# Optimization experiments

Hardware: AMD Instinct MI355X
Metric: run time of the kernel (lower is better)

Reference implementation:

```python
import jax, jax.numpy as jnp
import numpy as np

N = 160000   # active voxels
C = 64       # embed_channels
K = 2048     # clusters per level
G = 128      # voxel grid side (grid_size)
NEG = 0.01   # LeakyReLU negative slope (torch default)
EPS_BN = 1e-5


def _build_neighbors():
    # Random unique active voxels in a G^3 grid; 27-neighborhood index map for SubMConv3d.
    rng = np.random.default_rng(0)
    codes = np.sort(rng.choice(G ** 3, size=N, replace=False))
    xc = codes // (G * G); yc = (codes // G) % G; zc = codes % G
    nbrs = []
    for dx in (-1, 0, 1):
        for dy in (-1, 0, 1):
            for dz in (-1, 0, 1):
                nx, ny, nz = xc + dx, yc + dy, zc + dz
                inb = (nx >= 0) & (nx < G) & (ny >= 0) & (ny < G) & (nz >= 0) & (nz < G)
                ncode = nx * (G * G) + ny * G + nz
                pos = np.searchsorted(codes, np.where(inb, ncode, 0))
                pos = np.clip(pos, 0, N - 1)
                found = inb & (codes[pos] == ncode)
                nbrs.append(np.where(found, pos, -1))
    return np.stack(nbrs).astype(np.int32)  # [27, N], -1 = no active neighbor


def setup_inputs():
    key = jax.random.key(0)
    def nrm(i, shape, s=0.05):
        return jax.random.normal(jax.random.fold_in(key, i), shape, jnp.float32) * s
    return {
        'feat': jax.random.normal(jax.random.fold_in(key, 0), (N, C), jnp.float32),
        'lw_W': nrm(1, (3, C, C)), 'lw_g': jnp.ones((3, C)), 'lw_b': jnp.zeros((3, C)),
        'w_W': nrm(2, (3, C, C)),
        'proj_W': nrm(3, (4, C, C)), 'proj_g': jnp.ones((4, C)), 'proj_b': jnp.zeros((4, C)),
        'adaptive_W': nrm(4, (C, 3)),
        'fuse_W': nrm(5, (2 * C, C)), 'fuse_g': jnp.ones((C,)), 'fuse_b': jnp.zeros((C,)),
        'conv1_W': nrm(6, (27, C, C)), 'bn1_g': jnp.ones((C,)), 'bn1_b': jnp.zeros((C,)),
        'conv2_W': nrm(7, (27, C, C)), 'bn2_g': jnp.ones((C,)), 'bn2_b': jnp.zeros((C,)),
        'clusters': jax.random.randint(jax.random.fold_in(key, 8), (3, N), 0, K, dtype=jnp.int32),
        'nbr': jnp.asarray(_build_neighbors()),
    }


def _bn(x, g, b):
    # BatchNorm1d, training-mode (biased batch stats over N)
    m = x.mean(0)
    v = x.var(0)
    return (x - m) * jax.lax.rsqrt(v + EPS_BN) * g + b


def _lrelu(x):
    return jax.nn.leaky_relu(x, NEG)


def _seg_sum(x, seg):
    return jax.ops.segment_sum(x, seg, num_segments=K)


def _subm_conv(f, nbr, W):
    # Submanifold 3x3x3 conv: per kernel offset, masked gather + [C,C] matmul.
    out = jnp.zeros((f.shape[0], W.shape[-1]), f.dtype)
    for k in range(27):
        idx = nbr[k]
        g = jnp.where((idx >= 0)[:, None], f[jnp.maximum(idx, 0)], 0.0)
        out = out + g @ W[k]
    return out


def reference(feat, lw_W, lw_g, lw_b, w_W, proj_W, proj_g, proj_b, adaptive_W,
              fuse_W, fuse_g, fuse_b, conv1_W, bn1_g, bn1_b, conv2_W, bn2_g, bn2_b,
              clusters, nbr):
    feats = []
    for i in range(3):  # depth-1 cluster levels
        c = clusters[i]
        cnt = jnp.clip(_seg_sum(jnp.ones((feat.shape[0], 1), feat.dtype), c), 1.0, None)
        pw = _lrelu(_bn(feat @ lw_W[i], lw_g[i], lw_b[i]))
        pw = pw - (_seg_sum(pw, c) / cnt)[c]          # center by cluster mean
        pw = pw @ w_W[i]
        pw = jnp.exp(pw - pw.max())                    # global-max-stabilized exp
        pw = pw / (_seg_sum(pw, c)[c] + 1e-6)          # per-cluster softmax
        pfeat = _lrelu(_bn(feat @ proj_W[i], proj_g[i], proj_b[i])) * pw
        feats.append(_seg_sum(pfeat, c)[c])            # pool then broadcast back
    adp = jax.nn.softmax(feat @ adaptive_W, axis=1)    # [N, 3]
    feats = jnp.stack(feats, axis=1)                   # [N, 3, C]
    feats = jnp.einsum('ln,lnc->lc', adp, feats)
    f = _lrelu(_bn(feat @ proj_W[3], proj_g[3], proj_b[3]))
    f = jnp.concatenate([f, feats], axis=1)
    f = _lrelu(_bn(f @ fuse_W, fuse_g, fuse_b)) + feat
    res = f
    v = _lrelu(_bn(_subm_conv(f, nbr, conv1_W), bn1_g, bn1_b))
    v = _bn(_subm_conv(v, nbr, conv2_W), bn2_g, bn2_b)
    return _lrelu(v + res)
```

## Files before the change

### kernel.cpp

```cpp
#include <hip/hip_runtime.h>
#include <hip/hip_bf16.h>
#include <math.h>

#define KCL 2048
#define LRELU_NEG 0.01f
#define EPSBN 1e-5f

using s8v = __attribute__((ext_vector_type(8))) short;
using f4v = __attribute__((ext_vector_type(4))) float;

union U8 { ushort u[8]; uint4 v; };

__device__ __forceinline__ float lrelu(float x) { return x > 0.f ? x : LRELU_NEG * x; }
__device__ __forceinline__ ushort f2bf(float f) {
    __hip_bfloat16 h = __float2bfloat16(f);
    return *reinterpret_cast<ushort*>(&h);
}
__device__ __forceinline__ float bf2f(ushort u) { return __uint_as_float(((unsigned)u) << 16); }

__device__ __forceinline__ unsigned encf(float f) {
    unsigned u = __float_as_uint(f);
    return (u & 0x80000000u) ? ~u : (u | 0x80000000u);
}
__device__ __forceinline__ float decf(unsigned u) {
    return __uint_as_float((u & 0x80000000u) ? (u & 0x7fffffffu) : ~u);
}

__device__ __forceinline__ void bn_sb(const double* __restrict__ stats, const float* __restrict__ g,
                                      const float* __restrict__ b, int n, float* sb) {
    int t = threadIdx.x;
    if (t < 64) {
        float mean = (float)(stats[t] / n);
        float ex2 = (float)(stats[64 + t] / n);
        float var = fmaxf(ex2 - mean * mean, 0.f);
        float rstd = rsqrtf(var + EPSBN);
        float sc = rstd * g[t];
        sb[t] = sc;
        sb[64 + t] = b[t] - mean * sc;
    }
    __syncthreads();
}

__device__ __forceinline__ void mfma_tile(const uint4* As, const uint4* Ws, int rowA0, int rowA1,
                                          int swA0, int swA1, int l15, int lg, f4v acc[2][4]) {
    const s8v* Av = (const s8v*)As;
    const s8v* Wv = (const s8v*)Ws;
#pragma unroll
    for (int kb = 0; kb < 2; ++kb) {
        int gch = kb * 4 + lg;
        s8v a0 = Av[rowA0 * 8 + (gch ^ swA0)];
        s8v a1 = Av[rowA1 * 8 + (gch ^ swA1)];
#pragma unroll
        for (int nf = 0; nf < 4; ++nf) {
            int col = nf * 16 + l15;
            s8v bf = Wv[col * 8 + (gch ^ (col & 7))];
            acc[0][nf] = __builtin_amdgcn_mfma_f32_16x16x32_bf16(a0, bf, acc[0][nf], 0, 0, 0);
            acc[1][nf] = __builtin_amdgcn_mfma_f32_16x16x32_bf16(a1, bf, acc[1][nf], 0, 0, 0);
        }
    }
}

__device__ __forceinline__ void stage_w(const ushort* Wmat, uint4* Ws, int wrow, int wq) {
    const uint4* src = (const uint4*)(Wmat + (size_t)wrow * 64);
    int sw = wrow & 7;
    Ws[wrow * 8 + (wq ^ sw)] = src[wq];
    Ws[wrow * 8 + ((wq + 4) ^ sw)] = src[wq + 4];
}

__device__ __forceinline__ void stage_a_bf16(const ushort* S, uint4* As, int row, int n, int arow, int ah) {
    uint4 c0 = {0, 0, 0, 0}, c1 = c0, c2 = c0, c3 = c0;
    if (row < n) {
        const uint4* s = (const uint4*)(S + (size_t)row * 64) + ah * 4;
        c0 = s[0]; c1 = s[1]; c2 = s[2]; c3 = s[3];
    }
    int sw = arow & 7;
    uint4* dst = As + arow * 8;
    dst[(ah * 4 + 0) ^ sw] = c0;
    dst[(ah * 4 + 1) ^ sw] = c1;
    dst[(ah * 4 + 2) ^ sw] = c2;
    dst[(ah * 4 + 3) ^ sw] = c3;
}

__device__ __forceinline__ void stage_a_vals(const float* vals, uint4* As, int arow, int ah) {
    int sw = arow & 7;
    uint4* dst = As + arow * 8;
#pragma unroll
    for (int c = 0; c < 4; ++c) {
        U8 u;
#pragma unroll
        for (int e = 0; e < 8; ++e) u.u[e] = f2bf(vals[c * 8 + e]);
        dst[(ah * 4 + c) ^ sw] = u.v;
    }
}

__global__ __launch_bounds__(256) void prep_wt64(const float* __restrict__ lw, const float* __restrict__ wW,
                                                 const float* __restrict__ proj, const float* __restrict__ c1,
                                                 const float* __restrict__ c2, ushort* __restrict__ wt) {
    int bk = blockIdx.x;
    const float* W;
    if (bk < 3) W = lw + (size_t)bk * 4096;
    else if (bk < 6) W = wW + (size_t)(bk - 3) * 4096;
    else if (bk < 10) W = proj + (size_t)(bk - 6) * 4096;
    else if (bk < 37) W = c1 + (size_t)(bk - 10) * 4096;
    else W = c2 + (size_t)(bk - 37) * 4096;
    ushort* o = wt + (size_t)bk * 4096;
    for (int i = threadIdx.x; i < 4096; i += 256) {
        int kk = i >> 6, cc = i & 63;
        o[cc * 64 + kk] = f2bf(W[i]);
    }
}

__global__ __launch_bounds__(256) void prep_fuse(const float* __restrict__ Wf, ushort* __restrict__ o) {
    for (int i = threadIdx.x; i < 8192; i += 256) {
        int kk = i >> 6, cc = i & 63;
        o[cc * 128 + kk] = f2bf(Wf[i]);
    }
}

__global__ __launch_bounds__(256) void cvt_bf16_kernel(const float* __restrict__ in, ushort* __restrict__ o,
                                                       long n4) {
    for (long i = (long)blockIdx.x * 256 + threadIdx.x; i < n4; i += (long)gridDim.x * 256) {
        float4 x = ((const float4*)in)[i];
        ushort4 u;
        u.x = f2bf(x.x); u.y = f2bf(x.y); u.z = f2bf(x.z); u.w = f2bf(x.w);
        ((ushort4*)o)[i] = u;
    }
}

__global__ __launch_bounds__(256) void hist3_kernel(const int* __restrict__ clusters, int* __restrict__ cnt,
                                                    int n) {
    __shared__ int h[KCL];
    int l = blockIdx.x % 3;
    int nb = gridDim.x / 3, bi = blockIdx.x / 3;
    for (int i = threadIdx.x; i < KCL; i += 256) h[i] = 0;
    __syncthreads();
    const int* cl = clusters + (size_t)l * n;
    for (long i = (long)bi * 256 + threadIdx.x; i < n; i += (long)nb * 256)
        atomicAdd(&h[cl[i]], 1);
    __syncthreads();
    for (int i = threadIdx.x; i < KCL; i += 256) {
        int v = h[i];
        if (v) atomicAdd(&cnt[l * KCL + i], v);
    }
}

__global__ __launch_bounds__(256) void scan_kernel(const int* __restrict__ cnt, int* __restrict__ off,
                                                   int* __restrict__ cursor, int n) {
    int l = blockIdx.x;
    const int* c = cnt + l * KCL;
    __shared__ int part[256];
    __shared__ int pref[256];
    int t = threadIdx.x;
    int base = t * 8;
    int v[8];
    int s = 0;
#pragma unroll
    for (int j = 0; j < 8; ++j) { v[j] = c[base + j]; s += v[j]; }
    part[t] = s;
    __syncthreads();
    if (t == 0) {
        int acc = 0;
        for (int i = 0; i < 256; ++i) { pref[i] = acc; acc += part[i]; }
    }
    __syncthreads();
    int acc = pref[t] + l * n;
#pragma unroll
    for (int j = 0; j < 8; ++j) {
        off[l * KCL + base + j] = acc;
        cursor[l * KCL + base + j] = acc;
        acc += v[j];
    }
}

__global__ __launch_bounds__(256) void scatter_kernel(const int* __restrict__ clusters, int* __restrict__ cursor,
                                                      int* __restrict__ perm, int n) {
    long n3 = (long)n * 3;
    for (long i = (long)blockIdx.x * 256 + threadIdx.x; i < n3; i += (long)gridDim.x * 256) {
        int l = (i >= n) + (i >= 2 * (long)n);
        int c = clusters[i];
        int pos = atomicAdd(&cursor[l * KCL + c], 1);
        perm[pos] = (int)(i - (long)l * n);
    }
}

__global__ __launch_bounds__(256) void adp_kernel(const ushort* __restrict__ feat16, const float* __restrict__ aW,
                                                  float* __restrict__ adp, int n) {
    __shared__ float w[192];
    for (int i = threadIdx.x; i < 192; i += 256) w[i] = aW[i];
    __syncthreads();
    for (long row = (long)blockIdx.x * 256 + threadIdx.x; row < n; row += (long)gridDim.x * 256) {
        const ushort4* fr = (const ushort4*)(feat16 + row * 64);
        float l0 = 0.f, l1 = 0.f, l2 = 0.f;
#pragma unroll
        for (int q = 0; q < 16; ++q) {
            ushort4 uv = fr[q];
            float x0 = bf2f(uv.x), x1 = bf2f(uv.y), x2 = bf2f(uv.z), x3 = bf2f(uv.w);
            int k = q * 4;
            l0 += x0 * w[k * 3 + 0] + x1 * w[k * 3 + 3] + x2 * w[k * 3 + 6] + x3 * w[k * 3 + 9];
            l1 += x0 * w[k * 3 + 1] + x1 * w[k * 3 + 4] + x2 * w[k * 3 + 7] + x3 * w[k * 3 + 10];
            l2 += x0 * w[k * 3 + 2] + x1 * w[k * 3 + 5] + x2 * w[k * 3 + 8] + x3 * w[k * 3 + 11];
        }
        float m = fmaxf(l0, fmaxf(l1, l2));
        float e0 = expf(l0 - m), e1 = expf(l1 - m), e2 = expf(l2 - m);
        float inv = 1.f / (e0 + e1 + e2);
        adp[row * 3 + 0] = e0 * inv;
        adp[row * 3 + 1] = e1 * inv;
        adp[row * 3 + 2] = e2 * inv;
    }
}

__global__ __launch_bounds__(256) void lw3_gemm(const ushort* __restrict__ feat16, const ushort* __restrict__ lwW16,
                                                ushort* __restrict__ A3, int n, double* __restrict__ stats) {
    __shared__ uint4 As[128 * 8];
    __shared__ uint4 Ws[64 * 8];
    __shared__ float red[512];
    int t = threadIdx.x, lane = t & 63, w = t >> 6;
    int rb = blockIdx.x * 128;
    int arow = t >> 1, ah = t & 1;
    int wrow = t >> 2, wq = t & 3;
    const int l15 = lane & 15, lg = lane >> 4;
    int rowA0 = w * 32 + l15, rowA1 = rowA0 + 16;
    int swA0 = rowA0 & 7, swA1 = rowA1 & 7;
    int base = rb + w * 32;

    stage_a_bf16(feat16, As, rb + arow, n, arow, ah);

    for (int j = 0; j < 3; ++j) {
        stage_w(lwW16 + (size_t)j * 4096, Ws, wrow, wq);
        __syncthreads();
        f4v acc[2][4];
#pragma unroll
        for (int rf = 0; rf < 2; ++rf)
#pragma unroll
            for (int nf = 0; nf < 4; ++nf)
#pragma unroll
                for (int q = 0; q < 4; ++q) acc[rf][nf][q] = 0.f;
        mfma_tile(As, Ws, rowA0, rowA1, swA0, swA1, l15, lg, acc);
        ushort* out = A3 + (size_t)j * n * 64;
#pragma unroll
        for (int rf = 0; rf < 2; ++rf)
#pragma unroll
            for (int nf = 0; nf < 4; ++nf)
#pragma unroll
                for (int q = 0; q < 4; ++q) {
                    int r = base + rf * 16 + lg * 4 + q;
                    if (r < n) out[(size_t)r * 64 + nf * 16 + l15] = f2bf(acc[rf][nf][q]);
                }
#pragma unroll
        for (int nf = 0; nf < 4; ++nf) {
            float s = 0.f, s2 = 0.f;
#pragma unroll
            for (int rf = 0; rf < 2; ++rf)
#pragma unroll
                for (int q = 0; q < 4; ++q) {
                    int r = base + rf * 16 + lg * 4 + q;
                    if (r < n) {
                        float v = acc[rf][nf][q];
                        s += v;
                        s2 += v * v;
                    }
                }
            s += __shfl_xor(s, 16); s += __shfl_xor(s, 32);
            s2 += __shfl_xor(s2, 16); s2 += __shfl_xor(s2, 32);
            if (lg == 0) {
                red[w * 64 + nf * 16 + l15] = s;
                red[256 + w * 64 + nf * 16 + l15] = s2;
            }
        }
        __syncthreads();
        if (t < 64) {
            float s = red[t] + red[64 + t] + red[128 + t] + red[192 + t];
            float s2 = red[256 + t] + red[320 + t] + red[384 + t] + red[448 + t];
            double* st = stats + (size_t)(2 * j) * 128;
            atomicAdd(&st[t], (double)s);
            atomicAdd(&st[64 + t], (double)s2);
        }
    }
}

__global__ __launch_bounds__(256) void gemm_stats_bf16out(const ushort* __restrict__ src,
                                                          const ushort* __restrict__ Wt,
                                                          ushort* __restrict__ out, int n,
                                                          double* __restrict__ stats_out) {
    __shared__ uint4 As[128 * 8];
    __shared__ uint4 Ws[64 * 8];
    int t = threadIdx.x, lane = t & 63, w = t >> 6;
    int rb = blockIdx.x * 128;
    int arow = t >> 1, ah = t & 1;
    int wrow = t >> 2, wq = t & 3;
    const int l15 = lane & 15, lg = lane >> 4;
    stage_w(Wt, Ws, wrow, wq);
    stage_a_bf16(src, As, rb + arow, n, arow, ah);
    __syncthreads();
    f4v acc[2][4];
#pragma unroll
    for (int rf = 0; rf < 2; ++rf)
#pragma unroll
        for (int nf = 0; nf < 4; ++nf)
#pragma unroll
            for (int q = 0; q < 4; ++q) acc[rf][nf][q] = 0.f;
    int rowA0 = w * 32 + l15, rowA1 = rowA0 + 16;
    mfma_tile(As, Ws, rowA0, rowA1, rowA0 & 7, rowA1 & 7, l15, lg, acc);
    int base = rb + w * 32;
#pragma unroll
    for (int rf = 0; rf < 2; ++rf)
#pragma unroll
        for (int nf = 0; nf < 4; ++nf)
#pragma unroll
            for (int q = 0; q < 4; ++q) {
                int r = base + rf * 16 + lg * 4 + q;
                if (r < n) out[(size_t)r * 64 + nf * 16 + l15] = f2bf(acc[rf][nf][q]);
            }
    __syncthreads();
    float* sp = (float*)As;
    int gidx = w * 4 + lg;
#pragma unroll
    for (int nf = 0; nf < 4; ++nf) {
        int col = nf * 16 + l15;
        float s = 0.f, s2 = 0.f;
#pragma unroll
        for (int rf = 0; rf < 2; ++rf)
#pragma unroll
            for (int q = 0; q < 4; ++q) {
                int r = base + rf * 16 + lg * 4 + q;
                if (r < n) {
                    float v = acc[rf][nf][q];
                    s += v;
                    s2 += v * v;
                }
            }
        sp[gidx * 64 + col] = s;
        sp[1024 + gidx * 64 + col] = s2;
    }
    __syncthreads();
    if (t < 64) {
        float s = 0.f, s2 = 0.f;
#pragma unroll
        for (int i = 0; i < 16; ++i) {
            s += sp[i * 64 + t];
            s2 += sp[1024 + i * 64 + t];
        }
        atomicAdd(&stats_out[t], (double)s);
        atomicAdd(&stats_out[64 + t], (double)s2);
    }
}

__global__ __launch_bounds__(256) void reduce_mean3_kernel(const ushort* __restrict__ A3,
                                                           const double* __restrict__ stats,
                                                           const float* __restrict__ lw_g,
                                                           const float* __restrict__ lw_b, int n,
                                                           const int* __restrict__ cnts, const int* __restrict__ offs,
                                                           const int* __restrict__ perm,
                                                           float* __restrict__ meanB3) {
    int l = blockIdx.x >> 11, c = blockIdx.x & (KCL - 1);
    const ushort* A = A3 + (size_t)l * n * 64;
    __shared__ float sb[128];
    bn_sb(stats + (size_t)(2 * l) * 128, lw_g + l * 64, lw_b + l * 64, n, sb);
    int t = threadIdx.x, col = t & 63, rg = t >> 6;
    int o = offs[l * KCL + c], m = cnts[l * KCL + c];
    float acc = 0.f;
    float sc = sb[col], bi = sb[64 + col];
    for (int j = rg; j < m; j += 4) {
        int row = perm[o + j];
        acc += lrelu(bf2f(A[(size_t)row * 64 + col]) * sc + bi);
    }
    __shared__ float red[256];
    red[t] = acc;
    __syncthreads();
    if (t < 64) {
        float s = red[t] + red[t + 64] + red[t + 128] + red[t + 192];
        float cf = (float)m;
        if (cf < 1.f) cf = 1.f;
        meanB3[(size_t)l * KCL * 64 + (size_t)c * 64 + col] = s / cf;
    }
}

__global__ __launch_bounds__(256) void mw3_gemm(const float* __restrict__ meanB3, const ushort* __restrict__ wW16,
                                                float* __restrict__ MW3) {
    __shared__ uint4 As[128 * 8];
    __shared__ uint4 Ws[64 * 8];
    int l = blockIdx.x >> 4, b = blockIdx.x & 15;
    const float* src = meanB3 + (size_t)l * KCL * 64;
    float* out = MW3 + (size_t)l * KCL * 64;
    int t = threadIdx.x, lane = t & 63, w = t >> 6;
    int rb = b * 128;
    int arow = t >> 1, ah = t & 1;
    int wrow = t >> 2, wq = t & 3;
    const int l15 = lane & 15, lg = lane >> 4;
    stage_w(wW16 + (size_t)l * 4096, Ws, wrow, wq);
    {
        float vals[32];
        const float4* s = (const float4*)(src + (size_t)(rb + arow) * 64 + ah * 32);
#pragma unroll
        for (int q = 0; q < 8; ++q) {
            float4 x = s[q];
            vals[q * 4 + 0] = x.x; vals[q * 4 + 1] = x.y;
            vals[q * 4 + 2] = x.z; vals[q * 4 + 3] = x.w;
        }
        stage_a_vals(vals, As, arow, ah);
    }
    __syncthreads();
    f4v acc[2][4];
#pragma unroll
    for (int rf = 0; rf < 2; ++rf)
#pragma unroll
        for (int nf = 0; nf < 4; ++nf)
#pragma unroll
            for (int q = 0; q < 4; ++q) acc[rf][nf][q] = 0.f;
    int rowA0 = w * 32 + l15, rowA1 = rowA0 + 16;
    mfma_tile(As, Ws, rowA0, rowA1, rowA0 & 7, rowA1 & 7, l15, lg, acc);
    int base = rb + w * 32;
#pragma unroll
    for (int rf = 0; rf < 2; ++rf)
#pragma unroll
        for (int nf = 0; nf < 4; ++nf)
#pragma unroll
            for (int q = 0; q < 4; ++q) {
                int r = base + rf * 16 + lg * 4 + q;
                out[(size_t)r * 64 + nf * 16 + l15] = acc[rf][nf][q];
            }
}

__global__ __launch_bounds__(256) void cgemm3(const ushort* __restrict__ A3, const ushort* __restrict__ wW16,
                                              const float* __restrict__ MW3, const int* __restrict__ clusters,
                                              const double* __restrict__ stats, const float* __restrict__ lw_g,
                                              const float* __restrict__ lw_b, ushort* __restrict__ C3,
                                              unsigned* __restrict__ gmax, int n, int nb) {
    __shared__ uint4 As[128 * 8];
    __shared__ uint4 Ws[64 * 8];
    __shared__ float sb[128];
    int l = blockIdx.x / nb, b = blockIdx.x % nb;
    const ushort* A = A3 + (size_t)l * n * 64;
    ushort* C = C3 + (size_t)l * n * 64;
    const float* MW = MW3 + (size_t)l * KCL * 64;
    const int* clus = clusters + (size_t)l * n;
    int t = threadIdx.x, lane = t & 63, w = t >> 6;
    int rb = b * 128;
    int arow = t >> 1, ah = t & 1;
    int wrow = t >> 2, wq = t & 3;
    const int l15 = lane & 15, lg = lane >> 4;

    bn_sb(stats + (size_t)(2 * l) * 128, lw_g + l * 64, lw_b + l * 64, n, sb);
    stage_w(wW16 + (size_t)l * 4096, Ws, wrow, wq);
    {
        int row = rb + arow;
        float vals[32];
        if (row < n) {
            const U8* s8p = (const U8*)(A + (size_t)row * 64 + ah * 32);
#pragma unroll
            for (int c = 0; c < 4; ++c) {
                U8 u = s8p[c];
#pragma unroll
                for (int e = 0; e < 8; ++e) {
                    int col = ah * 32 + c * 8 + e;
                    vals[c * 8 + e] = lrelu(bf2f(u.u[e]) * sb[col] + sb[64 + col]);
                }
            }
        } else {
#pragma unroll
            for (int i = 0; i < 32; ++i) vals[i] = 0.f;
        }
        stage_a_vals(vals, As, arow, ah);
    }
    __syncthreads();
    f4v acc[2][4];
#pragma unroll
    for (int rf = 0; rf < 2; ++rf)
#pragma unroll
        for (int nf = 0; nf < 4; ++nf)
#pragma unroll
            for (int q = 0; q < 4; ++q) acc[rf][nf][q] = 0.f;
    int rowA0 = w * 32 + l15, rowA1 = rowA0 + 16;
    mfma_tile(As, Ws, rowA0, rowA1, rowA0 & 7, rowA1 & 7, l15, lg, acc);
    int base = rb + w * 32;
    float m = -INFINITY;
#pragma unroll
    for (int rf = 0; rf < 2; ++rf)
#pragma unroll
        for (int q = 0; q < 4; ++q) {
            int r = base + rf * 16 + lg * 4 + q;
            if (r < n) {
                int c = clus[r];
                const float* mwr = MW + (size_t)c * 64;
#pragma unroll
                for (int nf = 0; nf < 4; ++nf) {
                    int col = nf * 16 + l15;
                    float v = acc[rf][nf][q] - mwr[col];
                    C[(size_t)r * 64 + col] = f2bf(v);
                    m = fmaxf(m, v);
                }
            }
        }
    __syncthreads();
    float* sp = (float*)As;
    sp[t] = m;
    __syncthreads();
    for (int s = 128; s > 0; s >>= 1) {
        if (t < s) sp[t] = fmaxf(sp[t], sp[t + s]);
        __syncthreads();
    }
    if (t == 0) atomicMax(&gmax[l], encf(sp[0]));
}

__global__ __launch_bounds__(256) void reduce_expf_kernel(const ushort* __restrict__ C, const ushort* __restrict__ E,
                                                          const double* __restrict__ stats,
                                                          const float* __restrict__ g, const float* __restrict__ b,
                                                          int n, const unsigned* __restrict__ gmaxp,
                                                          const int* __restrict__ cnt, const int* __restrict__ off,
                                                          const int* __restrict__ perm, float* __restrict__ seg3) {
    __shared__ float sb[128];
    bn_sb(stats, g, b, n, sb);
    int c = blockIdx.x;
    int t = threadIdx.x, col = t & 63, rg = t >> 6;
    float gm = decf(*gmaxp);
    int o = off[c], m = cnt[c];
    float accd = 0.f, accn = 0.f;
    float sc = sb[col], bi = sb[64 + col];
    for (int j = rg; j < m; j += 4) {
        int row = perm[o + j];
        float d = expf(bf2f(C[(size_t)row * 64 + col]) - gm);
        float pf = lrelu(bf2f(E[(size_t)row * 64 + col]) * sc + bi);
        accd += d;
        accn += pf * d;
    }
    __shared__ float redd[256], redn[256];
    redd[t] = accd;
    redn[t] = accn;
    __syncthreads();
    if (t < 64) {
        float sd = redd[t] + redd[t + 64] + redd[t + 128] + redd[t + 192];
        float sn = redn[t] + redn[t + 64] + redn[t + 128] + redn[t + 192];
        seg3[(size_t)c * 64 + col] = sn / (sd + 1e-6f);
    }
}

__global__ __launch_bounds__(256) void fuse_mfma(const ushort* __restrict__ P3, const double* __restrict__ statsP,
                                                 const float* __restrict__ gg, const float* __restrict__ bb, int n,
                                                 const float* __restrict__ adp, const int* __restrict__ clusters,
                                                 const float* __restrict__ s3_0, const float* __restrict__ s3_1,
                                                 const float* __restrict__ s3_2, const ushort* __restrict__ WfT,
                                                 ushort* __restrict__ out, double* __restrict__ stats_out) {
    __shared__ uint4 As[128 * 8];
    __shared__ uint4 Ws[64 * 8];
    __shared__ float sb[128];
    int t = threadIdx.x, lane = t & 63, w = t >> 6;
    int rb = blockIdx.x * 128;
    int arow = t >> 1, ah = t & 1;
    int wrow = t >> 2, wq = t & 3;
    const int l15 = lane & 15, lg = lane >> 4;

    bn_sb(statsP, gg, bb, n, sb);

    f4v acc[2][4];
#pragma unroll
    for (int rf = 0; rf < 2; ++rf)
#pragma unroll
        for (int nf = 0; nf < 4; ++nf)
#pragma unroll
            for (int q = 0; q < 4; ++q) acc[rf][nf][q] = 0.f;

    int rowA0 = w * 32 + l15, rowA1 = rowA0 + 16;
    int row = rb + arow;

    for (int p = 0; p < 2; ++p) {
        if (p) __syncthreads();
        float vals[32];
        if (row < n) {
            if (p == 0) {
                const U8* s8p = (const U8*)(P3 + (size_t)row * 64 + ah * 32);
#pragma unroll
                for (int c = 0; c < 4; ++c) {
                    U8 u = s8p[c];
#pragma unroll
                    for (int e = 0; e < 8; ++e) {
                        int col = ah * 32 + c * 8 + e;
                        vals[c * 8 + e] = lrelu(bf2f(u.u[e]) * sb[col] + sb[64 + col]);
                    }
                }
            } else {
                float a0 = adp[(size_t)row * 3 + 0], a1 = adp[(size_t)row * 3 + 1], a2 = adp[(size_t)row * 3 + 2];
                const float* r0 = s3_0 + (size_t)clusters[row] * 64 + ah * 32;
                const float* r1 = s3_1 + (size_t)clusters[(size_t)n + row] * 64 + ah * 32;
                const float* r2 = s3_2 + (size_t)clusters[2 * (size_t)n + row] * 64 + ah * 32;
#pragma unroll
                for (int i = 0; i < 32; ++i) vals[i] = a0 * r0[i] + a1 * r1[i] + a2 * r2[i];
            }
        } else {
#pragma unroll
            for (int i = 0; i < 32; ++i) vals[i] = 0.f;
        }
        stage_a_vals(vals, As, arow, ah);
        {
            const uint4* srcw = (const uint4*)(WfT + (size_t)wrow * 128);
            int sw = wrow & 7;
            uint4* dst = Ws + wrow * 8;
            dst[wq ^ sw] = srcw[p * 8 + wq];
            dst[(wq + 4) ^ sw] = srcw[p * 8 + wq + 4];
        }
        __syncthreads();
        mfma_tile(As, Ws, rowA0, rowA1, rowA0 & 7, rowA1 & 7, l15, lg, acc);
    }
    int base = rb + w * 32;
#pragma unroll
    for (int rf = 0; rf < 2; ++rf)
#pragma unroll
        for (int nf = 0; nf < 4; ++nf)
#pragma unroll
            for (int q = 0; q < 4; ++q) {
                int r = base + rf * 16 + lg * 4 + q;
                if (r < n) out[(size_t)r * 64 + nf * 16 + l15] = f2bf(acc[rf][nf][q]);
            }
    __syncthreads();
    float* sp = (float*)As;
    int gidx = w * 4 + lg;
#pragma unroll
    for (int nf = 0; nf < 4; ++nf) {
        int col = nf * 16 + l15;
        float s = 0.f, s2 = 0.f;
#pragma unroll
        for (int rf = 0; rf < 2; ++rf)
#pragma unroll
            for (int q = 0; q < 4; ++q) {
                int r = base + rf * 16 + lg * 4 + q;
                if (r < n) {
                    float v = acc[rf][nf][q];
                    s += v;
                    s2 += v * v;
                }
            }
        sp[gidx * 64 + col] = s;
        sp[1024 + gidx * 64 + col] = s2;
    }
    __syncthreads();
    if (t < 64) {
        float s = 0.f, s2 = 0.f;
#pragma unroll
        for (int i = 0; i < 16; ++i) {
            s += sp[i * 64 + t];
            s2 += sp[1024 + i * 64 + t];
        }
        atomicAdd(&stats_out[t], (double)s);
        atomicAdd(&stats_out[64 + t], (double)s2);
    }
}

__global__ __launch_bounds__(256) void subm_conv_db(const ushort* __restrict__ fin, const int* __restrict__ nbr,
                                                    const ushort* __restrict__ Wt, ushort* __restrict__ vout,
                                                    int n, double* __restrict__ stats_out) {
    __shared__ uint4 As[2][128 * 8];
    __shared__ uint4 Ws[2][64 * 8];
    int t = threadIdx.x;
    int lane = t & 63, w = t >> 6;
    int rb = blockIdx.x * 128;
    int arow = t >> 1, ah = t & 1;
    int wrow = t >> 2, wq = t & 3;
    const int l15 = lane & 15, lg = lane >> 4;
    int rowA0 = w * 32 + l15, rowA1 = rowA0 + 16;
    int swA0 = rowA0 & 7, swA1 = rowA1 & 7;
    const bool rowok = (rb + arow) < n;
    const int swa = arow & 7, sww = wrow & 7;

    f4v acc[2][4];
#pragma unroll
    for (int rf = 0; rf < 2; ++rf)
#pragma unroll
        for (int nf = 0; nf < 4; ++nf)
#pragma unroll
            for (int q = 0; q < 4; ++q) acc[rf][nf][q] = 0.f;

    {
        int gi = rowok ? nbr[rb + arow] : -1;
        uint4 v0 = {0, 0, 0, 0}, v1 = v0, v2 = v0, v3 = v0;
        if (gi >= 0) {
            const uint4* src = (const uint4*)(fin + (size_t)gi * 64) + ah * 4;
            v0 = src[0]; v1 = src[1]; v2 = src[2]; v3 = src[3];
        }
        uint4* dst = As[0] + arow * 8;
        dst[(ah * 4 + 0) ^ swa] = v0;
        dst[(ah * 4 + 1) ^ swa] = v1;
        dst[(ah * 4 + 2) ^ swa] = v2;
        dst[(ah * 4 + 3) ^ swa] = v3;
        const uint4* ws = (const uint4*)(Wt + (size_t)wrow * 64);
        uint4* wdst = Ws[0] + wrow * 8;
        wdst[wq ^ sww] = ws[wq];
        wdst[(wq + 4) ^ sww] = ws[wq + 4];
    }
    int gi_next = rowok ? nbr[(size_t)n + rb + arow] : -1;
    int cur = 0;

    for (int k = 0; k < 27; ++k) {
        uint4 a0, a1, a2, a3, w0, w1;
        if (k < 26) {
            a0 = a1 = a2 = a3 = (uint4){0, 0, 0, 0};
            if (gi_next >= 0) {
                const uint4* src = (const uint4*)(fin + (size_t)gi_next * 64) + ah * 4;
                a0 = src[0]; a1 = src[1]; a2 = src[2]; a3 = src[3];
            }
            const uint4* ws = (const uint4*)(Wt + (size_t)(k + 1) * 4096 + (size_t)wrow * 64);
            w0 = ws[wq];
            w1 = ws[wq + 4];
            if (k < 25) gi_next = rowok ? nbr[(size_t)(k + 2) * n + rb + arow] : -1;
        }
        __syncthreads();
        mfma_tile(As[cur], Ws[cur], rowA0, rowA1, swA0, swA1, l15, lg, acc);
        if (k < 26) {
            uint4* dst = As[cur ^ 1] + arow * 8;
            dst[(ah * 4 + 0) ^ swa] = a0;
            dst[(ah * 4 + 1) ^ swa] = a1;
            dst[(ah * 4 + 2) ^ swa] = a2;
            dst[(ah * 4 + 3) ^ swa] = a3;
            uint4* wdst = Ws[cur ^ 1] + wrow * 8;
            wdst[wq ^ sww] = w0;
            wdst[(wq + 4) ^ sww] = w1;
            cur ^= 1;
        }
    }
    int base = rb + w * 32;
#pragma unroll
    for (int rf = 0; rf < 2; ++rf)
#pragma unroll
        for (int nf = 0; nf < 4; ++nf)
#pragma unroll
            for (int q = 0; q < 4; ++q) {
                int r = base + rf * 16 + lg * 4 + q;
                if (r < n) vout[(size_t)r * 64 + nf * 16 + l15] = f2bf(acc[rf][nf][q]);
            }
    __syncthreads();
    float* sp = (float*)As[0];
    int gidx = w * 4 + lg;
#pragma unroll
    for (int nf = 0; nf < 4; ++nf) {
        int col = nf * 16 + l15;
        float s = 0.f, s2 = 0.f;
#pragma unroll
        for (int rf = 0; rf < 2; ++rf)
#pragma unroll
            for (int q = 0; q < 4; ++q) {
                int r = base + rf * 16 + lg * 4 + q;
                if (r < n) {
                    float v = acc[rf][nf][q];
                    s += v;
                    s2 += v * v;
                }
            }
        sp[gidx * 64 + col] = s;
        sp[1024 + gidx * 64 + col] = s2;
    }
    __syncthreads();
    if (t < 64) {
        float s = 0.f, s2 = 0.f;
#pragma unroll
        for (int i = 0; i < 16; ++i) {
            s += sp[i * 64 + t];
            s2 += sp[1024 + i * 64 + t];
        }
        atomicAdd(&stats_out[t], (double)s);
        atomicAdd(&stats_out[64 + t], (double)s2);
    }
}

__global__ __launch_bounds__(256) void addfeat_kernel(const ushort* __restrict__ t3, const double* __restrict__ stats,
                                                      const float* __restrict__ g, const float* __restrict__ b,
                                                      const float* __restrict__ feat, ushort* __restrict__ f16,
                                                      int n) {
    __shared__ float sb[128];
    bn_sb(stats, g, b, n, sb);
    long total4 = (long)n * 16;
    for (long i = (long)blockIdx.x * 256 + threadIdx.x; i < total4; i += (long)gridDim.x * 256) {
        int c0 = (int)(i & 15) * 4;
        ushort4 xv = ((const ushort4*)t3)[i];
        float4 fz = ((const float4*)feat)[i];
        ushort4 u;
        u.x = f2bf(lrelu(bf2f(xv.x) * sb[c0 + 0] + sb[64 + c0 + 0]) + fz.x);
        u.y = f2bf(lrelu(bf2f(xv.y) * sb[c0 + 1] + sb[64 + c0 + 1]) + fz.y);
        u.z = f2bf(lrelu(bf2f(xv.z) * sb[c0 + 2] + sb[64 + c0 + 2]) + fz.z);
        u.w = f2bf(lrelu(bf2f(xv.w) * sb[c0 + 3] + sb[64 + c0 + 3]) + fz.w);
        ((ushort4*)f16)[i] = u;
    }
}

__global__ __launch_bounds__(256) void bnlrelu_tobf16_kernel(const ushort* __restrict__ v,
                                                             const double* __restrict__ stats,
                                                             const float* __restrict__ g, const float* __restrict__ b,
                                                             ushort* __restrict__ o16, int n) {
    __shared__ float sb[128];
    bn_sb(stats, g, b, n, sb);
    long total4 = (long)n * 16;
    for (long i = (long)blockIdx.x * 256 + threadIdx.x; i < total4; i += (long)gridDim.x * 256) {
        int c0 = (int)(i & 15) * 4;
        ushort4 xv = ((const ushort4*)v)[i];
        ushort4 u;
        u.x = f2bf(lrelu(bf2f(xv.x) * sb[c0 + 0] + sb[64 + c0 + 0]));
        u.y = f2bf(lrelu(bf2f(xv.y) * sb[c0 + 1] + sb[64 + c0 + 1]));
        u.z = f2bf(lrelu(bf2f(xv.z) * sb[c0 + 2] + sb[64 + c0 + 2]));
        u.w = f2bf(lrelu(bf2f(xv.w) * sb[c0 + 3] + sb[64 + c0 + 3]));
        ((ushort4*)o16)[i] = u;
    }
}

__global__ __launch_bounds__(256) void final_kernel(const ushort* __restrict__ w16, const double* __restrict__ stats,
                                                    const float* __restrict__ g, const float* __restrict__ b,
                                                    const ushort* __restrict__ f16, float* __restrict__ out, int n) {
    __shared__ float sb[128];
    bn_sb(stats, g, b, n, sb);
    long total4 = (long)n * 16;
    for (long i = (long)blockIdx.x * 256 + threadIdx.x; i < total4; i += (long)gridDim.x * 256) {
        int c0 = (int)(i & 15) * 4;
        ushort4 xv = ((const ushort4*)w16)[i];
        ushort4 u = ((const ushort4*)f16)[i];
        float4 y;
        y.x = lrelu(bf2f(xv.x) * sb[c0 + 0] + sb[64 + c0 + 0] + bf2f(u.x));
        y.y = lrelu(bf2f(xv.y) * sb[c0 + 1] + sb[64 + c0 + 1] + bf2f(u.y));
        y.z = lrelu(bf2f(xv.z) * sb[c0 + 2] + sb[64 + c0 + 2] + bf2f(u.z));
        y.w = lrelu(bf2f(xv.w) * sb[c0 + 3] + sb[64 + c0 + 3] + bf2f(u.w));
        ((float4*)out)[i] = y;
    }
}

extern "C" void kernel_launch(void* const* d_in, const int* in_sizes, int n_in,
                              void* d_out, int out_size, void* d_ws, size_t ws_size,
                              hipStream_t stream) {
    const float* feat = (const float*)d_in[0];
    const float* lw_W = (const float*)d_in[1];
    const float* lw_g = (const float*)d_in[2];
    const float* lw_b = (const float*)d_in[3];
    const float* w_W = (const float*)d_in[4];
    const float* proj_W = (const float*)d_in[5];
    const float* proj_g = (const float*)d_in[6];
    const float* proj_b = (const float*)d_in[7];
    const float* adaptive_W = (const float*)d_in[8];
    const float* fuse_W = (const float*)d_in[9];
    const float* fuse_g = (const float*)d_in[10];
    const float* fuse_b = (const float*)d_in[11];
    const float* conv1_W = (const float*)d_in[12];
    const float* bn1_g = (const float*)d_in[13];
    const float* bn1_b = (const float*)d_in[14];
    const float* conv2_W = (const float*)d_in[15];
    const float* bn2_g = (const float*)d_in[16];
    const float* bn2_b = (const float*)d_in[17];
    const int* clusters = (const int*)d_in[18];
    const int* nbr = (const int*)d_in[19];

    const int n = in_sizes[0] / 64;

    char* ws = (char*)d_ws;
    size_t off = 0;
    auto alloc = [&](size_t bytes) -> size_t {
        size_t o = off;
        off = (off + bytes + 255) & ~(size_t)255;
        return o;
    };
    size_t cnt_off = alloc((size_t)3 * KCL * 4);
    size_t stats_off = alloc((size_t)10 * 128 * 8);
    size_t gmax_off = alloc(16);
    size_t zbytes = off;
    size_t offs_off = alloc((size_t)3 * KCL * 4);
    size_t cur_off = alloc((size_t)3 * KCL * 4);
    size_t perm_off = alloc((size_t)3 * n * 4);
    size_t mean_off = alloc((size_t)3 * KCL * 64 * 4);
    size_t mw_off = alloc((size_t)3 * KCL * 64 * 4);
    size_t seg3_off = alloc((size_t)3 * KCL * 64 * 4);
    size_t adp_off = alloc((size_t)n * 3 * 4);
    size_t feat16_off = alloc((size_t)n * 64 * 2);
    size_t ra_off = alloc((size_t)3 * n * 64 * 2);
    size_t rc_off = alloc((size_t)3 * n * 64 * 2);
    size_t wt64_off = alloc((size_t)64 * 4096 * 2);
    size_t wfT_off = alloc((size_t)8192 * 2);

    int* cnts = (int*)(ws + cnt_off);
    double* stats = (double*)(ws + stats_off);
    unsigned* gmax = (unsigned*)(ws + gmax_off);
    int* offs = (int*)(ws + offs_off);
    int* cursor = (int*)(ws + cur_off);
    int* perm = (int*)(ws + perm_off);
    float* meanB3 = (float*)(ws + mean_off);
    float* MW3 = (float*)(ws + mw_off);
    float* seg3 = (float*)(ws + seg3_off);
    float* adp = (float*)(ws + adp_off);
    ushort* feat16 = (ushort*)(ws + feat16_off);
    ushort* RA = (ushort*)(ws + ra_off);
    ushort* RC = (ushort*)(ws + rc_off);
    ushort* wt64 = (ushort*)(ws + wt64_off);
    ushort* wfT = (ushort*)(ws + wfT_off);
    float* outp = (float*)d_out;

    ushort* A3 = RA;
    ushort* Ebuf = RA;
    ushort* c1out = RA + (size_t)n * 64;
    ushort* cbuf = RA + (size_t)2 * n * 64;
    ushort* c2out = RA;
    ushort* C3 = RC;
    ushort* P3buf = RC;
    ushort* t3buf = RC + (size_t)n * 64;
    ushort* fbuf16 = RC + (size_t)2 * n * 64;

    const ushort* lwW16 = wt64;
    const ushort* wW16 = wt64 + (size_t)3 * 4096;
    const ushort* projW16 = wt64 + (size_t)6 * 4096;
    const ushort* conv1W16 = wt64 + (size_t)10 * 4096;
    const ushort* conv2W16 = wt64 + (size_t)37 * 4096;

    hipMemsetAsync(d_ws, 0, zbytes, stream);

    const int GEMM_BLK = (n + 127) / 128;
    const int EW_BLK = 2048;

    prep_wt64<<<64, 256, 0, stream>>>(lw_W, w_W, proj_W, conv1_W, conv2_W, wt64);
    prep_fuse<<<1, 256, 0, stream>>>(fuse_W, wfT);
    cvt_bf16_kernel<<<EW_BLK, 256, 0, stream>>>(feat, feat16, (long)n * 16);
    adp_kernel<<<1024, 256, 0, stream>>>(feat16, adaptive_W, adp, n);

    hist3_kernel<<<384, 256, 0, stream>>>(clusters, cnts, n);
    scan_kernel<<<3, 256, 0, stream>>>(cnts, offs, cursor, n);
    scatter_kernel<<<1024, 256, 0, stream>>>(clusters, cursor, perm, n);

    lw3_gemm<<<GEMM_BLK, 256, 0, stream>>>(feat16, lwW16, A3, n, stats);
    reduce_mean3_kernel<<<3 * KCL, 256, 0, stream>>>(A3, stats, lw_g, lw_b, n, cnts, offs, perm, meanB3);
    mw3_gemm<<<3 * 16, 256, 0, stream>>>(meanB3, wW16, MW3);
    cgemm3<<<3 * GEMM_BLK, 256, 0, stream>>>(A3, wW16, MW3, clusters, stats, lw_g, lw_b, C3, gmax, n, GEMM_BLK);

    for (int i = 0; i < 3; ++i) {
        gemm_stats_bf16out<<<GEMM_BLK, 256, 0, stream>>>(feat16, projW16 + (size_t)i * 4096, Ebuf, n,
                                                         stats + (size_t)(2 * i + 1) * 128);
        reduce_expf_kernel<<<KCL, 256, 0, stream>>>(C3 + (size_t)i * n * 64, Ebuf,
                                                    stats + (size_t)(2 * i + 1) * 128,
                                                    proj_g + i * 64, proj_b + i * 64, n, gmax + i,
                                                    cnts + (size_t)i * KCL, offs + (size_t)i * KCL, perm,
                                                    seg3 + (size_t)i * KCL * 64);
    }

    gemm_stats_bf16out<<<GEMM_BLK, 256, 0, stream>>>(feat16, projW16 + (size_t)3 * 4096, P3buf, n,
                                                     stats + (size_t)6 * 128);
    fuse_mfma<<<GEMM_BLK, 256, 0, stream>>>(P3buf, stats + 6 * 128, proj_g + 192, proj_b + 192, n,
                                            adp, clusters,
                                            seg3, seg3 + (size_t)KCL * 64, seg3 + (size_t)2 * KCL * 64,
                                            wfT, t3buf, stats + 7 * 128);
    addfeat_kernel<<<EW_BLK, 256, 0, stream>>>(t3buf, stats + 7 * 128, fuse_g, fuse_b, feat, fbuf16, n);

    subm_conv_db<<<GEMM_BLK, 256, 0, stream>>>(fbuf16, nbr, conv1W16, c1out, n, stats + 8 * 128);
    bnlrelu_tobf16_kernel<<<EW_BLK, 256, 0, stream>>>(c1out, stats + 8 * 128, bn1_g, bn1_b, cbuf, n);

    subm_conv_db<<<GEMM_BLK, 256, 0, stream>>>(cbuf, nbr, conv2W16, c2out, n, stats + 9 * 128);
    final_kernel<<<EW_BLK, 256, 0, stream>>>(c2out, stats + 9 * 128, bn2_g, bn2_b, fbuf16, outp, n);
}
```

Before: 647.7 us.

## Fuse feat-side GEMMs into one kernel, batch expf pass, skip empty conv taps

Replaces the separate lw3 GEMM and four projection GEMMs with one kernel that stages the feat tile once and runs seven weight matrices against it. The three per-level softmax/pool passes become a single 3*KCL-block launch, and the feat conversion is folded into the adaptive-softmax kernel. Weight fragments are now read straight from global memory instead of being staged in shared memory. The submanifold conv uses wave ballots to skip MFMAs and LDS writes when a tap has no active neighbors. Buffers are reassigned, including using d_out as scratch, which adds aliasing risk.

```diff
diff --git a/kernel.cpp b/kernel.cpp
--- a/kernel.cpp
+++ b/kernel.cpp
@@ -41,10 +41,10 @@
     __syncthreads();
 }
 
-__device__ __forceinline__ void mfma_tile(const uint4* As, const uint4* Ws, int rowA0, int rowA1,
-                                          int swA0, int swA1, int l15, int lg, f4v acc[2][4]) {
+__device__ __forceinline__ void mfma_tileG(const uint4* As, const ushort* Wmat, int ws, int koff,
+                                           int rowA0, int rowA1, int swA0, int swA1,
+                                           int l15, int lg, f4v acc[2][4]) {
     const s8v* Av = (const s8v*)As;
-    const s8v* Wv = (const s8v*)Ws;
 #pragma unroll
     for (int kb = 0; kb < 2; ++kb) {
         int gch = kb * 4 + lg;
@@ -53,18 +53,11 @@
 #pragma unroll
         for (int nf = 0; nf < 4; ++nf) {
             int col = nf * 16 + l15;
-            s8v bf = Wv[col * 8 + (gch ^ (col & 7))];
+            s8v bf = *(const s8v*)(Wmat + (size_t)col * ws + koff + gch * 8);
             acc[0][nf] = __builtin_amdgcn_mfma_f32_16x16x32_bf16(a0, bf, acc[0][nf], 0, 0, 0);
             acc[1][nf] = __builtin_amdgcn_mfma_f32_16x16x32_bf16(a1, bf, acc[1][nf], 0, 0, 0);
         }
     }
-}
-
-__device__ __forceinline__ void stage_w(const ushort* Wmat, uint4* Ws, int wrow, int wq) {
-    const uint4* src = (const uint4*)(Wmat + (size_t)wrow * 64);
-    int sw = wrow & 7;
-    Ws[wrow * 8 + (wq ^ sw)] = src[wq];
-    Ws[wrow * 8 + ((wq + 4) ^ sw)] = src[wq + 4];
 }
 
 __device__ __forceinline__ void stage_a_bf16(const ushort* S, uint4* As, int row, int n, int arow, int ah) {
@@ -117,13 +110,32 @@
     }
 }
 
-__global__ __launch_bounds__(256) void cvt_bf16_kernel(const float* __restrict__ in, ushort* __restrict__ o,
-                                                       long n4) {
-    for (long i = (long)blockIdx.x * 256 + threadIdx.x; i < n4; i += (long)gridDim.x * 256) {
-        float4 x = ((const float4*)in)[i];
-        ushort4 u;
-        u.x = f2bf(x.x); u.y = f2bf(x.y); u.z = f2bf(x.z); u.w = f2bf(x.w);
-        ((ushort4*)o)[i] = u;
+__global__ __launch_bounds__(256) void adp_cvt_kernel(const float* __restrict__ feat, const float* __restrict__ aW,
+                                                      float* __restrict__ adp, ushort* __restrict__ feat16, int n) {
+    __shared__ float w[192];
+    for (int i = threadIdx.x; i < 192; i += 256) w[i] = aW[i];
+    __syncthreads();
+    for (long row = (long)blockIdx.x * 256 + threadIdx.x; row < n; row += (long)gridDim.x * 256) {
+        const float4* fr = (const float4*)(feat + row * 64);
+        ushort4* fo = (ushort4*)(feat16 + row * 64);
+        float l0 = 0.f, l1 = 0.f, l2 = 0.f;
+#pragma unroll
+        for (int q = 0; q < 16; ++q) {
+            float4 x = fr[q];
+            int k = q * 4;
+            l0 += x.x * w[k * 3 + 0] + x.y * w[k * 3 + 3] + x.z * w[k * 3 + 6] + x.w * w[k * 3 + 9];
+            l1 += x.x * w[k * 3 + 1] + x.y * w[k * 3 + 4] + x.z * w[k * 3 + 7] + x.w * w[k * 3 + 10];
+            l2 += x.x * w[k * 3 + 2] + x.y * w[k * 3 + 5] + x.z * w[k * 3 + 8] + x.w * w[k * 3 + 11];
+            ushort4 u;
+            u.x = f2bf(x.x); u.y = f2bf(x.y); u.z = f2bf(x.z); u.w = f2bf(x.w);
+            fo[q] = u;
+        }
+        float m = fmaxf(l0, fmaxf(l1, l2));
+        float e0 = expf(l0 - m), e1 = expf(l1 - m), e2 = expf(l2 - m);
+        float inv = 1.f / (e0 + e1 + e2);
+        adp[row * 3 + 0] = e0 * inv;
+        adp[row * 3 + 1] = e1 * inv;
+        adp[row * 3 + 2] = e2 * inv;
     }
 }
 
@@ -183,115 +195,10 @@
     }
 }
 
-__global__ __launch_bounds__(256) void adp_kernel(const ushort* __restrict__ feat16, const float* __restrict__ aW,
-                                                  float* __restrict__ adp, int n) {
-    __shared__ float w[192];
-    for (int i = threadIdx.x; i < 192; i += 256) w[i] = aW[i];
-    __syncthreads();
-    for (long row = (long)blockIdx.x * 256 + threadIdx.x; row < n; row += (long)gridDim.x * 256) {
-        const ushort4* fr = (const ushort4*)(feat16 + row * 64);
-        float l0 = 0.f, l1 = 0.f, l2 = 0.f;
-#pragma unroll
-        for (int q = 0; q < 16; ++q) {
-            ushort4 uv = fr[q];
-            float x0 = bf2f(uv.x), x1 = bf2f(uv.y), x2 = bf2f(uv.z), x3 = bf2f(uv.w);
-            int k = q * 4;
-            l0 += x0 * w[k * 3 + 0] + x1 * w[k * 3 + 3] + x2 * w[k * 3 + 6] + x3 * w[k * 3 + 9];
-            l1 += x0 * w[k * 3 + 1] + x1 * w[k * 3 + 4] + x2 * w[k * 3 + 7] + x3 * w[k * 3 + 10];
-            l2 += x0 * w[k * 3 + 2] + x1 * w[k * 3 + 5] + x2 * w[k * 3 + 8] + x3 * w[k * 3 + 11];
-        }
-        float m = fmaxf(l0, fmaxf(l1, l2));
-        float e0 = expf(l0 - m), e1 = expf(l1 - m), e2 = expf(l2 - m);
-        float inv = 1.f / (e0 + e1 + e2);
-        adp[row * 3 + 0] = e0 * inv;
-        adp[row * 3 + 1] = e1 * inv;
-        adp[row * 3 + 2] = e2 * inv;
-    }
-}
-
-__global__ __launch_bounds__(256) void lw3_gemm(const ushort* __restrict__ feat16, const ushort* __restrict__ lwW16,
-                                                ushort* __restrict__ A3, int n, double* __restrict__ stats) {
-    __shared__ uint4 As[128 * 8];
-    __shared__ uint4 Ws[64 * 8];
-    __shared__ float red[512];
-    int t = threadIdx.x, lane = t & 63, w = t >> 6;
-    int rb = blockIdx.x * 128;
-    int arow = t >> 1, ah = t & 1;
-    int wrow = t >> 2, wq = t & 3;
+__device__ __forceinline__ void mega_one(const uint4* As, float* red, const ushort* Wmat, ushort* out,
+                                         double* statp, int n, int rb, int w, int lane, int t) {
     const int l15 = lane & 15, lg = lane >> 4;
     int rowA0 = w * 32 + l15, rowA1 = rowA0 + 16;
-    int swA0 = rowA0 & 7, swA1 = rowA1 & 7;
-    int base = rb + w * 32;
-
-    stage_a_bf16(feat16, As, rb + arow, n, arow, ah);
-
-    for (int j = 0; j < 3; ++j) {
-        stage_w(lwW16 + (size_t)j * 4096, Ws, wrow, wq);
-        __syncthreads();
-        f4v acc[2][4];
-#pragma unroll
-        for (int rf = 0; rf < 2; ++rf)
-#pragma unroll
-            for (int nf = 0; nf < 4; ++nf)
-#pragma unroll
-                for (int q = 0; q < 4; ++q) acc[rf][nf][q] = 0.f;
-        mfma_tile(As, Ws, rowA0, rowA1, swA0, swA1, l15, lg, acc);
-        ushort* out = A3 + (size_t)j * n * 64;
-#pragma unroll
-        for (int rf = 0; rf < 2; ++rf)
-#pragma unroll
-            for (int nf = 0; nf < 4; ++nf)
-#pragma unroll
-                for (int q = 0; q < 4; ++q) {
-                    int r = base + rf * 16 + lg * 4 + q;
-                    if (r < n) out[(size_t)r * 64 + nf * 16 + l15] = f2bf(acc[rf][nf][q]);
-                }
-#pragma unroll
-        for (int nf = 0; nf < 4; ++nf) {
-            float s = 0.f, s2 = 0.f;
-#pragma unroll
-            for (int rf = 0; rf < 2; ++rf)
-#pragma unroll
-                for (int q = 0; q < 4; ++q) {
-                    int r = base + rf * 16 + lg * 4 + q;
-                    if (r < n) {
-                        float v = acc[rf][nf][q];
-                        s += v;
-                        s2 += v * v;
-                    }
-                }
-            s += __shfl_xor(s, 16); s += __shfl_xor(s, 32);
-            s2 += __shfl_xor(s2, 16); s2 += __shfl_xor(s2, 32);
-            if (lg == 0) {
-                red[w * 64 + nf * 16 + l15] = s;
-                red[256 + w * 64 + nf * 16 + l15] = s2;
-            }
-        }
-        __syncthreads();
-        if (t < 64) {
-            float s = red[t] + red[64 + t] + red[128 + t] + red[192 + t];
-            float s2 = red[256 + t] + red[320 + t] + red[384 + t] + red[448 + t];
-            double* st = stats + (size_t)(2 * j) * 128;
-            atomicAdd(&st[t], (double)s);
-            atomicAdd(&st[64 + t], (double)s2);
-        }
-    }
-}
-
-__global__ __launch_bounds__(256) void gemm_stats_bf16out(const ushort* __restrict__ src,
-                                                          const ushort* __restrict__ Wt,
-                                                          ushort* __restrict__ out, int n,
-                                                          double* __restrict__ stats_out) {
-    __shared__ uint4 As[128 * 8];
-    __shared__ uint4 Ws[64 * 8];
-    int t = threadIdx.x, lane = t & 63, w = t >> 6;
-    int rb = blockIdx.x * 128;
-    int arow = t >> 1, ah = t & 1;
-    int wrow = t >> 2, wq = t & 3;
-    const int l15 = lane & 15, lg = lane >> 4;
-    stage_w(Wt, Ws, wrow, wq);
-    stage_a_bf16(src, As, rb + arow, n, arow, ah);
-    __syncthreads();
     f4v acc[2][4];
 #pragma unroll
     for (int rf = 0; rf < 2; ++rf)
@@ -299,8 +206,7 @@
         for (int nf = 0; nf < 4; ++nf)
 #pragma unroll
             for (int q = 0; q < 4; ++q) acc[rf][nf][q] = 0.f;
-    int rowA0 = w * 32 + l15, rowA1 = rowA0 + 16;
-    mfma_tile(As, Ws, rowA0, rowA1, rowA0 & 7, rowA1 & 7, l15, lg, acc);
+    mfma_tileG(As, Wmat, 64, 0, rowA0, rowA1, rowA0 & 7, rowA1 & 7, l15, lg, acc);
     int base = rb + w * 32;
 #pragma unroll
     for (int rf = 0; rf < 2; ++rf)
@@ -311,12 +217,8 @@
                 int r = base + rf * 16 + lg * 4 + q;
                 if (r < n) out[(size_t)r * 64 + nf * 16 + l15] = f2bf(acc[rf][nf][q]);
             }
-    __syncthreads();
-    float* sp = (float*)As;
-    int gidx = w * 4 + lg;
 #pragma unroll
     for (int nf = 0; nf < 4; ++nf) {
-        int col = nf * 16 + l15;
         float s = 0.f, s2 = 0.f;
 #pragma unroll
         for (int rf = 0; rf < 2; ++rf)
@@ -329,20 +231,44 @@
                     s2 += v * v;
                 }
             }
-        sp[gidx * 64 + col] = s;
-        sp[1024 + gidx * 64 + col] = s2;
+        s += __shfl_xor(s, 16); s += __shfl_xor(s, 32);
+        s2 += __shfl_xor(s2, 16); s2 += __shfl_xor(s2, 32);
+        if (lg == 0) {
+            red[w * 64 + nf * 16 + l15] = s;
+            red[256 + w * 64 + nf * 16 + l15] = s2;
+        }
     }
     __syncthreads();
     if (t < 64) {
-        float s = 0.f, s2 = 0.f;
-#pragma unroll
-        for (int i = 0; i < 16; ++i) {
-            s += sp[i * 64 + t];
-            s2 += sp[1024 + i * 64 + t];
-        }
-        atomicAdd(&stats_out[t], (double)s);
-        atomicAdd(&stats_out[64 + t], (double)s2);
-    }
+        float s = red[t] + red[64 + t] + red[128 + t] + red[192 + t];
+        float s2 = red[256 + t] + red[320 + t] + red[384 + t] + red[448 + t];
+        atomicAdd(&statp[t], (double)s);
+        atomicAdd(&statp[64 + t], (double)s2);
+    }
+    __syncthreads();
+}
+
+__global__ __launch_bounds__(256) void mega7_gemm(const ushort* __restrict__ feat16,
+                                                  const ushort* __restrict__ wt64,
+                                                  ushort* __restrict__ o0, ushort* __restrict__ o1,
+                                                  ushort* __restrict__ o2, ushort* __restrict__ o3,
+                                                  ushort* __restrict__ o4, ushort* __restrict__ o5,
+                                                  ushort* __restrict__ o6,
+                                                  int n, double* __restrict__ stats) {
+    __shared__ uint4 As[128 * 8];
+    __shared__ float red[512];
+    int t = threadIdx.x, lane = t & 63, w = t >> 6;
+    int rb = blockIdx.x * 128;
+    int arow = t >> 1, ah = t & 1;
+    stage_a_bf16(feat16, As, rb + arow, n, arow, ah);
+    __syncthreads();
+    mega_one(As, red, wt64 + (size_t)0 * 4096, o0, stats + 0 * 128, n, rb, w, lane, t);
+    mega_one(As, red, wt64 + (size_t)1 * 4096, o1, stats + 2 * 128, n, rb, w, lane, t);
+    mega_one(As, red, wt64 + (size_t)2 * 4096, o2, stats + 4 * 128, n, rb, w, lane, t);
+    mega_one(As, red, wt64 + (size_t)6 * 4096, o3, stats + 1 * 128, n, rb, w, lane, t);
+    mega_one(As, red, wt64 + (size_t)7 * 4096, o4, stats + 3 * 128, n, rb, w, lane, t);
+    mega_one(As, red, wt64 + (size_t)8 * 4096, o5, stats + 5 * 128, n, rb, w, lane, t);
+    mega_one(As, red, wt64 + (size_t)9 * 4096, o6, stats + 6 * 128, n, rb, w, lane, t);
 }
 
 __global__ __launch_bounds__(256) void reduce_mean3_kernel(const ushort* __restrict__ A3,
@@ -378,16 +304,13 @@
 __global__ __launch_bounds__(256) void mw3_gemm(const float* __restrict__ meanB3, const ushort* __restrict__ wW16,
                                                 float* __restrict__ MW3) {
     __shared__ uint4 As[128 * 8];
-    __shared__ uint4 Ws[64 * 8];
     int l = blockIdx.x >> 4, b = blockIdx.x & 15;
     const float* src = meanB3 + (size_t)l * KCL * 64;
     float* out = MW3 + (size_t)l * KCL * 64;
     int t = threadIdx.x, lane = t & 63, w = t >> 6;
     int rb = b * 128;
     int arow = t >> 1, ah = t & 1;
-    int wrow = t >> 2, wq = t & 3;
     const int l15 = lane & 15, lg = lane >> 4;
-    stage_w(wW16 + (size_t)l * 4096, Ws, wrow, wq);
     {
         float vals[32];
         const float4* s = (const float4*)(src + (size_t)(rb + arow) * 64 + ah * 32);
@@ -408,7 +331,7 @@
 #pragma unroll
             for (int q = 0; q < 4; ++q) acc[rf][nf][q] = 0.f;
     int rowA0 = w * 32 + l15, rowA1 = rowA0 + 16;
-    mfma_tile(As, Ws, rowA0, rowA1, rowA0 & 7, rowA1 & 7, l15, lg, acc);
+    mfma_tileG(As, wW16 + (size_t)l * 4096, 64, 0, rowA0, rowA1, rowA0 & 7, rowA1 & 7, l15, lg, acc);
     int base = rb + w * 32;
 #pragma unroll
     for (int rf = 0; rf < 2; ++rf)
@@ -421,27 +344,23 @@
             }
 }
 
-__global__ __launch_bounds__(256) void cgemm3(const ushort* __restrict__ A3, const ushort* __restrict__ wW16,
+__global__ __launch_bounds__(256) void cgemm3(ushort* __restrict__ A3io, const ushort* __restrict__ wW16,
                                               const float* __restrict__ MW3, const int* __restrict__ clusters,
                                               const double* __restrict__ stats, const float* __restrict__ lw_g,
-                                              const float* __restrict__ lw_b, ushort* __restrict__ C3,
+                                              const float* __restrict__ lw_b,
                                               unsigned* __restrict__ gmax, int n, int nb) {
     __shared__ uint4 As[128 * 8];
-    __shared__ uint4 Ws[64 * 8];
     __shared__ float sb[128];
     int l = blockIdx.x / nb, b = blockIdx.x % nb;
-    const ushort* A = A3 + (size_t)l * n * 64;
-    ushort* C = C3 + (size_t)l * n * 64;
+    ushort* A = A3io + (size_t)l * n * 64;
     const float* MW = MW3 + (size_t)l * KCL * 64;
     const int* clus = clusters + (size_t)l * n;
     int t = threadIdx.x, lane = t & 63, w = t >> 6;
     int rb = b * 128;
     int arow = t >> 1, ah = t & 1;
-    int wrow = t >> 2, wq = t & 3;
     const int l15 = lane & 15, lg = lane >> 4;
 
     bn_sb(stats + (size_t)(2 * l) * 128, lw_g + l * 64, lw_b + l * 64, n, sb);
-    stage_w(wW16 + (size_t)l * 4096, Ws, wrow, wq);
     {
         int row = rb + arow;
         float vals[32];
@@ -471,7 +390,7 @@
 #pragma unroll
             for (int q = 0; q < 4; ++q) acc[rf][nf][q] = 0.f;
     int rowA0 = w * 32 + l15, rowA1 = rowA0 + 16;
-    mfma_tile(As, Ws, rowA0, rowA1, rowA0 & 7, rowA1 & 7, l15, lg, acc);
+    mfma_tileG(As, wW16 + (size_t)l * 4096, 64, 0, rowA0, rowA1, rowA0 & 7, rowA1 & 7, l15, lg, acc);
     int base = rb + w * 32;
     float m = -INFINITY;
 #pragma unroll
@@ -486,7 +405,7 @@
                 for (int nf = 0; nf < 4; ++nf) {
                     int col = nf * 16 + l15;
                     float v = acc[rf][nf][q] - mwr[col];
-                    C[(size_t)r * 64 + col] = f2bf(v);
+                    A[(size_t)r * 64 + col] = f2bf(v);
                     m = fmaxf(m, v);
                 }
             }
@@ -502,18 +421,21 @@
     if (t == 0) atomicMax(&gmax[l], encf(sp[0]));
 }
 
-__global__ __launch_bounds__(256) void reduce_expf_kernel(const ushort* __restrict__ C, const ushort* __restrict__ E,
-                                                          const double* __restrict__ stats,
-                                                          const float* __restrict__ g, const float* __restrict__ b,
-                                                          int n, const unsigned* __restrict__ gmaxp,
-                                                          const int* __restrict__ cnt, const int* __restrict__ off,
-                                                          const int* __restrict__ perm, float* __restrict__ seg3) {
+__global__ __launch_bounds__(256) void expf3_kernel(const ushort* __restrict__ C3, const ushort* __restrict__ E0,
+                                                    const ushort* __restrict__ E1, const ushort* __restrict__ E2,
+                                                    const double* __restrict__ stats,
+                                                    const float* __restrict__ proj_g, const float* __restrict__ proj_b,
+                                                    int n, const unsigned* __restrict__ gmax,
+                                                    const int* __restrict__ cnts, const int* __restrict__ offs,
+                                                    const int* __restrict__ perm, float* __restrict__ seg3) {
+    int l = blockIdx.x >> 11, c = blockIdx.x & (KCL - 1);
+    const ushort* C = C3 + (size_t)l * n * 64;
+    const ushort* E = (l == 0) ? E0 : (l == 1) ? E1 : E2;
     __shared__ float sb[128];
-    bn_sb(stats, g, b, n, sb);
-    int c = blockIdx.x;
+    bn_sb(stats + (size_t)(2 * l + 1) * 128, proj_g + l * 64, proj_b + l * 64, n, sb);
     int t = threadIdx.x, col = t & 63, rg = t >> 6;
-    float gm = decf(*gmaxp);
-    int o = off[c], m = cnt[c];
+    float gm = decf(gmax[l]);
+    int o = offs[l * KCL + c], m = cnts[l * KCL + c];
     float accd = 0.f, accn = 0.f;
     float sc = sb[col], bi = sb[64 + col];
     for (int j = rg; j < m; j += 4) {
@@ -530,7 +452,7 @@
     if (t < 64) {
         float sd = redd[t] + redd[t + 64] + redd[t + 128] + redd[t + 192];
         float sn = redn[t] + redn[t + 64] + redn[t + 128] + redn[t + 192];
-        seg3[(size_t)c * 64 + col] = sn / (sd + 1e-6f);
+        seg3[(size_t)l * KCL * 64 + (size_t)c * 64 + col] = sn / (sd + 1e-6f);
     }
 }
 
@@ -541,12 +463,10 @@
                                                  const float* __restrict__ s3_2, const ushort* __restrict__ WfT,
                                                  ushort* __restrict__ out, double* __restrict__ stats_out) {
     __shared__ uint4 As[128 * 8];
-    __shared__ uint4 Ws[64 * 8];
     __shared__ float sb[128];
     int t = threadIdx.x, lane = t & 63, w = t >> 6;
     int rb = blockIdx.x * 128;
     int arow = t >> 1, ah = t & 1;
-    int wrow = t >> 2, wq = t & 3;
     const int l15 = lane & 15, lg = lane >> 4;
 
     bn_sb(statsP, gg, bb, n, sb);
@@ -590,15 +510,8 @@
             for (int i = 0; i < 32; ++i) vals[i] = 0.f;
         }
         stage_a_vals(vals, As, arow, ah);
-        {
-            const uint4* srcw = (const uint4*)(WfT + (size_t)wrow * 128);
-            int sw = wrow & 7;
-            uint4* dst = Ws + wrow * 8;
-            dst[wq ^ sw] = srcw[p * 8 + wq];
-            dst[(wq + 4) ^ sw] = srcw[p * 8 + wq + 4];
-        }
         __syncthreads();
-        mfma_tile(As, Ws, rowA0, rowA1, rowA0 & 7, rowA1 & 7, l15, lg, acc);
+        mfma_tileG(As, WfT, 128, p * 64, rowA0, rowA1, rowA0 & 7, rowA1 & 7, l15, lg, acc);
     }
     int base = rb + w * 32;
 #pragma unroll
@@ -644,21 +557,21 @@
     }
 }
 
-__global__ __launch_bounds__(256) void subm_conv_db(const ushort* __restrict__ fin, const int* __restrict__ nbr,
-                                                    const ushort* __restrict__ Wt, ushort* __restrict__ vout,
-                                                    int n, double* __restrict__ stats_out) {
-    __shared__ uint4 As[2][128 * 8];
-    __shared__ uint4 Ws[2][64 * 8];
-    int t = threadIdx.x;
-    int lane = t & 63, w = t >> 6;
+__global__ __launch_bounds__(256) void subm_conv_g(const ushort* __restrict__ fin, const int* __restrict__ nbr,
+                                                   const ushort* __restrict__ Wt, ushort* __restrict__ vout,
+                                                   int n, double* __restrict__ stats_out) {
+    __shared__ uint4 AsBuf[2][128 * 8];
+    int t = threadIdx.x, lane = t & 63, w = t >> 6;
     int rb = blockIdx.x * 128;
     int arow = t >> 1, ah = t & 1;
-    int wrow = t >> 2, wq = t & 3;
     const int l15 = lane & 15, lg = lane >> 4;
     int rowA0 = w * 32 + l15, rowA1 = rowA0 + 16;
     int swA0 = rowA0 & 7, swA1 = rowA1 & 7;
     const bool rowok = (rb + arow) < n;
-    const int swa = arow & 7, sww = wrow & 7;
+    const int swa = arow & 7;
+
+    uint4* bufc = AsBuf[0];
+    uint4* bufn = AsBuf[1];
 
     f4v acc[2][4];
 #pragma unroll
@@ -668,51 +581,78 @@
 #pragma unroll
             for (int q = 0; q < 4; ++q) acc[rf][nf][q] = 0.f;
 
+    bool fc0, fc1, wzc, wzn = false;
     {
         int gi = rowok ? nbr[rb + arow] : -1;
         uint4 v0 = {0, 0, 0, 0}, v1 = v0, v2 = v0, v3 = v0;
         if (gi >= 0) {
-            const uint4* src = (const uint4*)(fin + (size_t)gi * 64) + ah * 4;
-            v0 = src[0]; v1 = src[1]; v2 = src[2]; v3 = src[3];
-        }
-        uint4* dst = As[0] + arow * 8;
+            const uint4* s = (const uint4*)(fin + (size_t)gi * 64) + ah * 4;
+            v0 = s[0]; v1 = s[1]; v2 = s[2]; v3 = s[3];
+        }
+        unsigned long long bal = __ballot(gi >= 0);
+        fc0 = (bal & 0xffffffffull) != 0ull;
+        fc1 = (bal >> 32) != 0ull;
+        wzc = (gi < 0);
+        uint4* dst = bufc + arow * 8;
         dst[(ah * 4 + 0) ^ swa] = v0;
         dst[(ah * 4 + 1) ^ swa] = v1;
         dst[(ah * 4 + 2) ^ swa] = v2;
         dst[(ah * 4 + 3) ^ swa] = v3;
-        const uint4* ws = (const uint4*)(Wt + (size_t)wrow * 64);
-        uint4* wdst = Ws[0] + wrow * 8;
-        wdst[wq ^ sww] = ws[wq];
-        wdst[(wq + 4) ^ sww] = ws[wq + 4];
-    }
-    int gi_next = rowok ? nbr[(size_t)n + rb + arow] : -1;
-    int cur = 0;
+    }
+    int gin = rowok ? nbr[(size_t)n + rb + arow] : -1;
 
     for (int k = 0; k < 27; ++k) {
-        uint4 a0, a1, a2, a3, w0, w1;
+        uint4 v0 = {0, 0, 0, 0}, v1 = v0, v2 = v0, v3 = v0;
+        bool fn0 = false, fn1 = false, missn = true;
         if (k < 26) {
-            a0 = a1 = a2 = a3 = (uint4){0, 0, 0, 0};
-            if (gi_next >= 0) {
-                const uint4* src = (const uint4*)(fin + (size_t)gi_next * 64) + ah * 4;
-                a0 = src[0]; a1 = src[1]; a2 = src[2]; a3 = src[3];
-            }
-            const uint4* ws = (const uint4*)(Wt + (size_t)(k + 1) * 4096 + (size_t)wrow * 64);
-            w0 = ws[wq];
-            w1 = ws[wq + 4];
-            if (k < 25) gi_next = rowok ? nbr[(size_t)(k + 2) * n + rb + arow] : -1;
+            missn = (gin < 0);
+            if (!missn) {
+                const uint4* s = (const uint4*)(fin + (size_t)gin * 64) + ah * 4;
+                v0 = s[0]; v1 = s[1]; v2 = s[2]; v3 = s[3];
+            }
+            unsigned long long bal = __ballot(!missn);
+            fn0 = (bal & 0xffffffffull) != 0ull;
+            fn1 = (bal >> 32) != 0ull;
+            if (k < 25) gin = rowok ? nbr[(size_t)(k + 2) * n + rb + arow] : -1;
         }
         __syncthreads();
-        mfma_tile(As[cur], Ws[cur], rowA0, rowA1, swA0, swA1, l15, lg, acc);
+        if (fc0 | fc1) {
+            const ushort* Wk = Wt + (size_t)k * 4096;
+            const s8v* Av = (const s8v*)bufc;
+#pragma unroll
+            for (int kb = 0; kb < 2; ++kb) {
+                int gch = kb * 4 + lg;
+                s8v bfr[4];
+#pragma unroll
+                for (int nf = 0; nf < 4; ++nf)
+                    bfr[nf] = *(const s8v*)(Wk + (size_t)(nf * 16 + l15) * 64 + gch * 8);
+                if (fc0) {
+                    s8v a0 = Av[rowA0 * 8 + (gch ^ swA0)];
+#pragma unroll
+                    for (int nf = 0; nf < 4; ++nf)
+                        acc[0][nf] = __builtin_amdgcn_mfma_f32_16x16x32_bf16(a0, bfr[nf], acc[0][nf], 0, 0, 0);
+                }
+                if (fc1) {
+                    s8v a1 = Av[rowA1 * 8 + (gch ^ swA1)];
+#pragma unroll
+                    for (int nf = 0; nf < 4; ++nf)
+                        acc[1][nf] = __builtin_amdgcn_mfma_f32_16x16x32_bf16(a1, bfr[nf], acc[1][nf], 0, 0, 0);
+                }
+            }
+        }
         if (k < 26) {
-            uint4* dst = As[cur ^ 1] + arow * 8;
-            dst[(ah * 4 + 0) ^ swa] = a0;
-            dst[(ah * 4 + 1) ^ swa] = a1;
-            dst[(ah * 4 + 2) ^ swa] = a2;
-            dst[(ah * 4 + 3) ^ swa] = a3;
-            uint4* wdst = Ws[cur ^ 1] + wrow * 8;
-            wdst[wq ^ sww] = w0;
-            wdst[(wq + 4) ^ sww] = w1;
-            cur ^= 1;
+            if (!(missn && wzn)) {
+                uint4* dst = bufn + arow * 8;
+                dst[(ah * 4 + 0) ^ swa] = v0;
+                dst[(ah * 4 + 1) ^ swa] = v1;
+                dst[(ah * 4 + 2) ^ swa] = v2;
+                dst[(ah * 4 + 3) ^ swa] = v3;
+            }
+            uint4* tb = bufc; bufc = bufn; bufn = tb;
+            bool nwzn = wzc;
+            wzc = missn;
+            wzn = nwzn;
+            fc0 = fn0; fc1 = fn1;
         }
     }
     int base = rb + w * 32;
@@ -726,7 +666,7 @@
                 if (r < n) vout[(size_t)r * 64 + nf * 16 + l15] = f2bf(acc[rf][nf][q]);
             }
     __syncthreads();
-    float* sp = (float*)As[0];
+    float* sp = (float*)AsBuf[0];
     int gidx = w * 4 + lg;
 #pragma unroll
     for (int nf = 0; nf < 4; ++nf) {
@@ -863,7 +803,7 @@
     size_t adp_off = alloc((size_t)n * 3 * 4);
     size_t feat16_off = alloc((size_t)n * 64 * 2);
     size_t ra_off = alloc((size_t)3 * n * 64 * 2);
-    size_t rc_off = alloc((size_t)3 * n * 64 * 2);
+    size_t re_off = alloc((size_t)2 * n * 64 * 2);
     size_t wt64_off = alloc((size_t)64 * 4096 * 2);
     size_t wfT_off = alloc((size_t)8192 * 2);
 
@@ -879,24 +819,23 @@
     float* adp = (float*)(ws + adp_off);
     ushort* feat16 = (ushort*)(ws + feat16_off);
     ushort* RA = (ushort*)(ws + ra_off);
-    ushort* RC = (ushort*)(ws + rc_off);
+    ushort* RE = (ushort*)(ws + re_off);
     ushort* wt64 = (ushort*)(ws + wt64_off);
     ushort* wfT = (ushort*)(ws + wfT_off);
     float* outp = (float*)d_out;
 
     ushort* A3 = RA;
-    ushort* Ebuf = RA;
-    ushort* c1out = RA + (size_t)n * 64;
-    ushort* cbuf = RA + (size_t)2 * n * 64;
-    ushort* c2out = RA;
-    ushort* C3 = RC;
-    ushort* P3buf = RC;
-    ushort* t3buf = RC + (size_t)n * 64;
-    ushort* fbuf16 = RC + (size_t)2 * n * 64;
-
-    const ushort* lwW16 = wt64;
+    ushort* E0 = RE;
+    ushort* E1 = RE + (size_t)n * 64;
+    ushort* E2 = (ushort*)d_out;
+    ushort* P3 = (ushort*)d_out + (size_t)n * 64;
+    ushort* t3buf = RA;
+    ushort* fbuf16 = RA + (size_t)n * 64;
+    ushort* c1out = RA + (size_t)2 * n * 64;
+    ushort* cbuf = RE;
+    ushort* c2out = RE + (size_t)n * 64;
+
     const ushort* wW16 = wt64 + (size_t)3 * 4096;
-    const ushort* projW16 = wt64 + (size_t)6 * 4096;
     const ushort* conv1W16 = wt64 + (size_t)10 * 4096;
     const ushort* conv2W16 = wt64 + (size_t)37 * 4096;
 
@@ -907,39 +846,30 @@
 
     prep_wt64<<<64, 256, 0, stream>>>(lw_W, w_W, proj_W, conv1_W, conv2_W, wt64);
     prep_fuse<<<1, 256, 0, stream>>>(fuse_W, wfT);
-    cvt_bf16_kernel<<<EW_BLK, 256, 0, stream>>>(feat, feat16, (long)n * 16);
-    adp_kernel<<<1024, 256, 0, stream>>>(feat16, adaptive_W, adp, n);
+    adp_cvt_kernel<<<1024, 256, 0, stream>>>(feat, adaptive_W, adp, feat16, n);
 
     hist3_kernel<<<384, 256, 0, stream>>>(clusters, cnts, n);
     scan_kernel<<<3, 256, 0, stream>>>(cnts, offs, cursor, n);
     scatter_kernel<<<1024, 256, 0, stream>>>(clusters, cursor, perm, n);
 
-    lw3_gemm<<<GEMM_BLK, 256, 0, stream>>>(feat16, lwW16, A3, n, stats);
+    mega7_gemm<<<GEMM_BLK, 256, 0, stream>>>(feat16, wt64,
+                                             A3, A3 + (size_t)n * 64, A3 + (size_t)2 * n * 64,
+                                             E0, E1, E2, P3, n, stats);
     reduce_mean3_kernel<<<3 * KCL, 256, 0, stream>>>(A3, stats, lw_g, lw_b, n, cnts, offs, perm, meanB3);
     mw3_gemm<<<3 * 16, 256, 0, stream>>>(meanB3, wW16, MW3);
-    cgemm3<<<3 * GEMM_BLK, 256, 0, stream>>>(A3, wW16, MW3, clusters, stats, lw_g, lw_b, C3, gmax, n, GEMM_BLK);
-
-    for (int i = 0; i < 3; ++i) {
-        gemm_stats_bf16out<<<GEMM_BLK, 256, 0, stream>>>(feat16, projW16 + (size_t)i * 4096, Ebuf, n,
-                                                         stats + (size_t)(2 * i + 1) * 128);
-        reduce_expf_kernel<<<KCL, 256, 0, stream>>>(C3 + (size_t)i * n * 64, Ebuf,
-                                                    stats + (size_t)(2 * i + 1) * 128,
-                                                    proj_g + i * 64, proj_b + i * 64, n, gmax + i,
-                                                    cnts + (size_t)i * KCL, offs + (size_t)i * KCL, perm,
-                                                    seg3 + (size_t)i * KCL * 64);
-    }
-
-    gemm_stats_bf16out<<<GEMM_BLK, 256, 0, stream>>>(feat16, projW16 + (size_t)3 * 4096, P3buf, n,
-                                                     stats + (size_t)6 * 128);
-    fuse_mfma<<<GEMM_BLK, 256, 0, stream>>>(P3buf, stats + 6 * 128, proj_g + 192, proj_b + 192, n,
+    cgemm3<<<3 * GEMM_BLK, 256, 0, stream>>>(A3, wW16, MW3, clusters, stats, lw_g, lw_b, gmax, n, GEMM_BLK);
+    expf3_kernel<<<3 * KCL, 256, 0, stream>>>(A3, E0, E1, E2, stats, proj_g, proj_b, n, gmax,
+                                              cnts, offs, perm, seg3);
+
+    fuse_mfma<<<GEMM_BLK, 256, 0, stream>>>(P3, stats + 6 * 128, proj_g + 192, proj_b + 192, n,
                                             adp, clusters,
                                             seg3, seg3 + (size_t)KCL * 64, seg3 + (size_t)2 * KCL * 64,
                                             wfT, t3buf, stats + 7 * 128);
     addfeat_kernel<<<EW_BLK, 256, 0, stream>>>(t3buf, stats + 7 * 128, fuse_g, fuse_b, feat, fbuf16, n);
 
-    subm_conv_db<<<GEMM_BLK, 256, 0, stream>>>(fbuf16, nbr, conv1W16, c1out, n, stats + 8 * 128);
+    subm_conv_g<<<GEMM_BLK, 256, 0, stream>>>(fbuf16, nbr, conv1W16, c1out, n, stats + 8 * 128);
     bnlrelu_tobf16_kernel<<<EW_BLK, 256, 0, stream>>>(c1out, stats + 8 * 128, bn1_g, bn1_b, cbuf, n);
 
-    subm_conv_db<<<GEMM_BLK, 256, 0, stream>>>(cbuf, nbr, conv2W16, c2out, n, stats + 9 * 128);
+    subm_conv_g<<<GEMM_BLK, 256, 0, stream>>>(cbuf, nbr, conv2W16, c2out, n, stats + 9 * 128);
     final_kernel<<<EW_BLK, 256, 0, stream>>>(c2out, stats + 9 * 128, bn2_g, bn2_b, fbuf16, outp, n);
 }
```

New measurement: 796.9 us. +23.0%, slower.
